# Optimization experiments

Hardware: AMD Instinct MI355X
Metric: run time of the kernel (lower is better)

The kernel has to match this reference:

```python
import jax, jax.numpy as jnp
import numpy as np

EPS = 1e-06        # normalize eps and log eps (module's self.eps)
PDIST_EPS = 1e-06  # torch.nn.PairwiseDistance default eps: ||x1 - x2 + eps||_2

A, C, F = 4096, 8, 64


def setup_inputs() -> dict:
    key = jax.random.key(0)
    x = jax.random.normal(key, (A, C, F), dtype=jnp.float32)
    return {"x": x}


def reference(x) -> jnp.ndarray:
    a = x.shape[0]
    c = x.shape[1]
    # F.normalize(p=2, dim=-1, eps=EPS): x / max(||x||_2, eps)
    nrm = jnp.linalg.norm(x, axis=-1, keepdims=True)
    xn = x / jnp.maximum(nrm, EPS)
    # pairwise cosine similarity per group: [C, A, A]
    sim = jnp.einsum('acf,bcf->cab', xn, xn)
    # mask self-similarity on the diagonal with -1
    diag = jnp.eye(a, dtype=bool)[None, :, :]
    sim = jnp.where(diag, -1.0, sim)
    # nearest neighbor per (c, a): argmax over b -> [C, A] -> [A, C]
    idx = jnp.argmax(sim, axis=-1).T
    # gather matched embeddings: x_match[a, c, f] = xn[idx[a, c], c, f]
    x_match = xn[idx, jnp.arange(c)[None, :], :]
    # PairwiseDistance(p=2, eps=1e-6): ||x - x_match + eps||_2 over last dim
    min_dist = jnp.linalg.norm(xn - x_match + PDIST_EPS, axis=-1)
    loss = -jnp.mean(jnp.log(min_dist + EPS))
    return loss
```

## Files before the change

### kernel.cpp

```cpp
#include <hip/hip_runtime.h>
#include <math.h>

#define AN 4096
#define CN 8
#define FN 64
#define ACN (AN*CN)

typedef __attribute__((ext_vector_type(8))) short bf16x8;
typedef __attribute__((ext_vector_type(4))) float f32x4;

__device__ inline unsigned short f2bf(float f) {
    unsigned u = __float_as_uint(f);
    unsigned r = ((u >> 16) & 1) + 0x7FFFu;
    return (unsigned short)((u + r) >> 16);
}

__global__ __launch_bounds__(256) void k1_normalize(const float* __restrict__ x,
                                                    float* __restrict__ xn,
                                                    unsigned short* __restrict__ xnb)
{
    int tid  = threadIdx.x;
    int grp  = tid >> 4;
    int slot = tid & 15;
    int V = blockIdx.x * 16 + grp;
    const float4 v = *(const float4*)(x + (size_t)V * FN + slot * 4);
    float ss = v.x*v.x + v.y*v.y + v.z*v.z + v.w*v.w;
    ss += __shfl_xor(ss, 1);
    ss += __shfl_xor(ss, 2);
    ss += __shfl_xor(ss, 4);
    ss += __shfl_xor(ss, 8);
    float sc = 1.0f / fmaxf(sqrtf(ss), 1e-6f);
    float4 o; o.x = v.x*sc; o.y = v.y*sc; o.z = v.z*sc; o.w = v.w*sc;
    *(float4*)(xn + (size_t)V * FN + slot * 4) = o;
    int a = V >> 3, c = V & 7;
    ushort4 ob;
    ob.x = f2bf(o.x); ob.y = f2bf(o.y); ob.z = f2bf(o.z); ob.w = f2bf(o.w);
    *(ushort4*)(xnb + ((size_t)c * AN + a) * FN + slot * 4) = ob;
}

__global__ __launch_bounds__(256, 2) void k2_argmax(const unsigned short* __restrict__ xnb,
                                                    unsigned int* __restrict__ pP)
{
    __shared__ uint4 lds4[3 * 1024];

    int blk  = blockIdx.x;
    int half = blk & 1;
    int rt   = (blk >> 1) & 31;
    int c    = blk >> 6;
    int a0   = rt * 128;
    int b0base = half * 2048;

    const uint4* __restrict__ Xc4 = (const uint4*)(xnb + (size_t)c * AN * FN);

    int tid  = threadIdx.x;
    int lane = tid & 63;
    int w    = tid >> 6;
    int wr   = w >> 1;
    int wc   = w & 1;
    int l15  = lane & 15;
    int quad = lane >> 4;

    int srow   = tid >> 3;
    int schunk = tid & 7;

    #pragma unroll
    for (int s = 0; s < 4; ++s) {
        int r = srow + 32 * s;
        lds4[r * 8 + (schunk ^ (r & 7))] = Xc4[(size_t)(a0 + r) * 8 + schunk];
    }
    #pragma unroll
    for (int s = 0; s < 4; ++s) {
        int r = srow + 32 * s;
        lds4[1024 + r * 8 + (schunk ^ (r & 7))] = Xc4[(size_t)(b0base + r) * 8 + schunk];
    }
    __syncthreads();

    bf16x8 afr[4][2];
    #pragma unroll
    for (int mi = 0; mi < 4; ++mi)
        #pragma unroll
        for (int ks = 0; ks < 2; ++ks) {
            int r  = wr * 64 + mi * 16 + l15;
            int ch = (ks * 4 + quad) ^ (r & 7);
            afr[mi][ks] = ((const bf16x8*)lds4)[r * 8 + ch];
        }

    float bestp[16];
    #pragma unroll
    for (int i = 0; i < 16; ++i) bestp[i] = 0.0f;

    const f32x4 two = {2.0f, 2.0f, 2.0f, 2.0f};

    for (int it = 0; it < 16; ++it) {
        int cur = it & 1;
        uint4 gv[4];
        if (it < 15) {
            int g0 = b0base + (it + 1) * 128;
            #pragma unroll
            for (int s = 0; s < 4; ++s)
                gv[s] = Xc4[(size_t)(g0 + srow + 32 * s) * 8 + schunk];
        }

        f32x4 acc[4][4];
        const bf16x8* bt = (const bf16x8*)(lds4 + 1024 + cur * 1024);
        #pragma unroll
        for (int ks = 0; ks < 2; ++ks) {
            #pragma unroll
            for (int ni = 0; ni < 4; ++ni) {
                int r  = wc * 64 + ni * 16 + l15;
                int ch = (ks * 4 + quad) ^ (r & 7);
                bf16x8 bfr = bt[r * 8 + ch];
                #pragma unroll
                for (int mi = 0; mi < 4; ++mi)
                    acc[mi][ni] = __builtin_amdgcn_mfma_f32_16x16x32_bf16(
                        afr[mi][ks], bfr, (ks == 0) ? two : acc[mi][ni], 0, 0, 0);
            }
        }

        int colblk = b0base + it * 128 + wc * 64;
        #pragma unroll
        for (int ni = 0; ni < 4; ++ni) {
            int cfrag = colblk + ni * 16;
            unsigned code = (unsigned)(cfrag + l15);
            #pragma unroll
            for (int mi = 0; mi < 4; ++mi) {
                int rfrag = a0 + wr * 64 + mi * 16;
                bool dg = (rfrag == cfrag);
                #pragma unroll
                for (int r = 0; r < 4; ++r) {
                    unsigned pb = (__float_as_uint(acc[mi][ni][r]) & 0xFFFFF000u) | code;
                    if (dg && (l15 == quad * 4 + r)) pb = 0u;
                    int bi = mi * 4 + r;
                    bestp[bi] = fmaxf(bestp[bi], __uint_as_float(pb));
                }
            }
        }

        if (it < 15) {
            #pragma unroll
            for (int s = 0; s < 4; ++s) {
                int r = srow + 32 * s;
                lds4[1024 + (cur ^ 1) * 1024 + r * 8 + (schunk ^ (r & 7))] = gv[s];
            }
        }
        __syncthreads();
    }

    #pragma unroll
    for (int i = 0; i < 16; ++i) {
        float v = bestp[i];
        v = fmaxf(v, __shfl_xor(v, 1));
        v = fmaxf(v, __shfl_xor(v, 2));
        v = fmaxf(v, __shfl_xor(v, 4));
        v = fmaxf(v, __shfl_xor(v, 8));
        bestp[i] = v;
    }
    __syncthreads();
    float* red = (float*)lds4;
    if (l15 == 0) {
        #pragma unroll
        for (int mi = 0; mi < 4; ++mi)
            #pragma unroll
            for (int r = 0; r < 4; ++r)
                red[w * 64 + mi * 16 + quad * 4 + r] = bestp[mi * 4 + r];
    }
    __syncthreads();
    if (tid < 128) {
        int wr2 = tid >> 6, r64 = tid & 63;
        float p = fmaxf(red[(2 * wr2) * 64 + r64], red[(2 * wr2 + 1) * 64 + r64]);
        int a = a0 + tid;
        pP[(size_t)half * ACN + (size_t)a * CN + c] = __float_as_uint(p);
    }
}

__global__ __launch_bounds__(256) void k3_dist(const float* __restrict__ xn,
                                               const unsigned int* __restrict__ pP,
                                               float* __restrict__ partials)
{
    int id = blockIdx.x * 256 + threadIdx.x;
    float p0 = __uint_as_float(pP[id]);
    float p1 = __uint_as_float(pP[ACN + id]);
    unsigned pm = __float_as_uint(fmaxf(p0, p1));
    int m = (int)(pm & 0xFFFu);
    int c = id & 7;
    const float* xa = xn + (size_t)id * FN;
    const float* xb = xn + ((size_t)m * CN + c) * FN;
    float ss = 0.0f;
    #pragma unroll
    for (int q = 0; q < 16; ++q) {
        float4 va = *(const float4*)(xa + 4 * q);
        float4 vb = *(const float4*)(xb + 4 * q);
        float d0 = va.x - vb.x + 1e-6f;
        float d1 = va.y - vb.y + 1e-6f;
        float d2 = va.z - vb.z + 1e-6f;
        float d3 = va.w - vb.w + 1e-6f;
        ss += d0*d0 + d1*d1 + d2*d2 + d3*d3;
    }
    float val = logf(sqrtf(ss) + 1e-6f);

    float t = val;
    #pragma unroll
    for (int off = 32; off > 0; off >>= 1) t += __shfl_down(t, off);
    __shared__ float ws4[4];
    if ((threadIdx.x & 63) == 0) ws4[threadIdx.x >> 6] = t;
    __syncthreads();
    if (threadIdx.x == 0)
        partials[blockIdx.x] = ws4[0] + ws4[1] + ws4[2] + ws4[3];
}

__global__ __launch_bounds__(64) void k4_final(const float* __restrict__ partials,
                                               float* __restrict__ out)
{
    int t = threadIdx.x;
    float v = partials[t] + partials[t + 64];
    #pragma unroll
    for (int off = 32; off > 0; off >>= 1) v += __shfl_down(v, off);
    if (t == 0) out[0] = -v / (float)ACN;
}

extern "C" void kernel_launch(void* const* d_in, const int* in_sizes, int n_in,
                              void* d_out, int out_size, void* d_ws, size_t ws_size,
                              hipStream_t stream)
{
    const float* x = (const float*)d_in[0];
    float* ws = (float*)d_ws;
    float* xn = ws;
    unsigned short* xnb = (unsigned short*)(xn + (size_t)AN * CN * FN);
    unsigned int* pP = (unsigned int*)(xnb + (size_t)AN * CN * FN);
    float* partials = (float*)(pP + 2 * ACN);

    k1_normalize<<<2048, 256, 0, stream>>>(x, xn, xnb);
    k2_argmax  <<<512, 256, 0, stream>>>(xnb, pP);
    k3_dist    <<<128, 256, 0, stream>>>(xn, pP, partials);
    k4_final   <<<1, 64, 0, stream>>>(partials, (float*)d_out);
}
```

Before: 93.57 us.

## Load MFMA operands straight from global memory and drop the fp32 normalized copy

The argmax kernel no longer stages tiles in LDS with double buffering and per-iteration barriers. Each wave now loads its A and B bf16 fragments directly from global memory (so via L1/L2), fully unrolls the column loop, and masks the diagonal only on the one iteration that holds it. The normalize kernel stops writing the fp32 normalized tensor and stores only a per-row scale, which the distance kernel applies to the raw input, cutting global write traffic. In exchange, B fragments are fetched redundantly from cache by several waves, and the fully unrolled loop raises register pressure.

```diff
diff --git a/kernel.cpp b/kernel.cpp
--- a/kernel.cpp
+++ b/kernel.cpp
@@ -16,8 +16,8 @@
 }
 
 __global__ __launch_bounds__(256) void k1_normalize(const float* __restrict__ x,
-                                                    float* __restrict__ xn,
-                                                    unsigned short* __restrict__ xnb)
+                                                    unsigned short* __restrict__ xnb,
+                                                    float* __restrict__ sc)
 {
     int tid  = threadIdx.x;
     int grp  = tid >> 4;
@@ -29,28 +29,24 @@
     ss += __shfl_xor(ss, 2);
     ss += __shfl_xor(ss, 4);
     ss += __shfl_xor(ss, 8);
-    float sc = 1.0f / fmaxf(sqrtf(ss), 1e-6f);
-    float4 o; o.x = v.x*sc; o.y = v.y*sc; o.z = v.z*sc; o.w = v.w*sc;
-    *(float4*)(xn + (size_t)V * FN + slot * 4) = o;
+    float s = 1.0f / fmaxf(sqrtf(ss), 1e-6f);
+    if (slot == 0) sc[V] = s;
+    ushort4 ob;
+    ob.x = f2bf(v.x * s); ob.y = f2bf(v.y * s);
+    ob.z = f2bf(v.z * s); ob.w = f2bf(v.w * s);
     int a = V >> 3, c = V & 7;
-    ushort4 ob;
-    ob.x = f2bf(o.x); ob.y = f2bf(o.y); ob.z = f2bf(o.z); ob.w = f2bf(o.w);
     *(ushort4*)(xnb + ((size_t)c * AN + a) * FN + slot * 4) = ob;
 }
 
 __global__ __launch_bounds__(256, 2) void k2_argmax(const unsigned short* __restrict__ xnb,
                                                     unsigned int* __restrict__ pP)
 {
-    __shared__ uint4 lds4[3 * 1024];
-
     int blk  = blockIdx.x;
     int half = blk & 1;
     int rt   = (blk >> 1) & 31;
     int c    = blk >> 6;
     int a0   = rt * 128;
     int b0base = half * 2048;
-
-    const uint4* __restrict__ Xc4 = (const uint4*)(xnb + (size_t)c * AN * FN);
 
     int tid  = threadIdx.x;
     int lane = tid & 63;
@@ -60,90 +56,67 @@
     int l15  = lane & 15;
     int quad = lane >> 4;
 
-    int srow   = tid >> 3;
-    int schunk = tid & 7;
-
-    #pragma unroll
-    for (int s = 0; s < 4; ++s) {
-        int r = srow + 32 * s;
-        lds4[r * 8 + (schunk ^ (r & 7))] = Xc4[(size_t)(a0 + r) * 8 + schunk];
-    }
-    #pragma unroll
-    for (int s = 0; s < 4; ++s) {
-        int r = srow + 32 * s;
-        lds4[1024 + r * 8 + (schunk ^ (r & 7))] = Xc4[(size_t)(b0base + r) * 8 + schunk];
-    }
-    __syncthreads();
-
+    const bf16x8* __restrict__ X8 = (const bf16x8*)(xnb + (size_t)c * AN * FN);
+
+    int arow = a0 + wr * 64 + l15;
     bf16x8 afr[4][2];
     #pragma unroll
     for (int mi = 0; mi < 4; ++mi)
         #pragma unroll
-        for (int ks = 0; ks < 2; ++ks) {
-            int r  = wr * 64 + mi * 16 + l15;
-            int ch = (ks * 4 + quad) ^ (r & 7);
-            afr[mi][ks] = ((const bf16x8*)lds4)[r * 8 + ch];
+        for (int ks = 0; ks < 2; ++ks)
+            afr[mi][ks] = X8[(size_t)(arow + mi * 16) * 8 + ks * 4 + quad];
+
+    int row0 = a0 + wr * 64;
+    int rel  = row0 - b0base;
+    int dit  = ((unsigned)rel < 2048u && (((rel >> 6) & 1) == wc)) ? (rel >> 7) : -1;
+    int sdit = __builtin_amdgcn_readfirstlane(dit);
+
+    float bestp[16];
+    #pragma unroll
+    for (int i = 0; i < 16; ++i) bestp[i] = 0.0f;
+
+    const f32x4 two = {2.0f, 2.0f, 2.0f, 2.0f};
+    int bcol = b0base + wc * 64 + l15;
+
+    #pragma unroll
+    for (int it = 0; it < 16; ++it) {
+        bf16x8 bfr[2][4];
+        #pragma unroll
+        for (int ks = 0; ks < 2; ++ks)
+            #pragma unroll
+            for (int ni = 0; ni < 4; ++ni)
+                bfr[ks][ni] = X8[(size_t)(bcol + it * 128 + ni * 16) * 8 + ks * 4 + quad];
+
+        f32x4 acc[4][4];
+        #pragma unroll
+        for (int ni = 0; ni < 4; ++ni)
+            #pragma unroll
+            for (int mi = 0; mi < 4; ++mi) {
+                acc[mi][ni] = __builtin_amdgcn_mfma_f32_16x16x32_bf16(afr[mi][0], bfr[0][ni], two, 0, 0, 0);
+                acc[mi][ni] = __builtin_amdgcn_mfma_f32_16x16x32_bf16(afr[mi][1], bfr[1][ni], acc[mi][ni], 0, 0, 0);
+            }
+
+        if (it == sdit) {
+            #pragma unroll
+            for (int mi = 0; mi < 4; ++mi)
+                #pragma unroll
+                for (int rr = 0; rr < 4; ++rr)
+                    if (l15 == quad * 4 + rr) acc[mi][mi][rr] = -2.0f;
         }
 
-    float bestp[16];
-    #pragma unroll
-    for (int i = 0; i < 16; ++i) bestp[i] = 0.0f;
-
-    const f32x4 two = {2.0f, 2.0f, 2.0f, 2.0f};
-
-    for (int it = 0; it < 16; ++it) {
-        int cur = it & 1;
-        uint4 gv[4];
-        if (it < 15) {
-            int g0 = b0base + (it + 1) * 128;
-            #pragma unroll
-            for (int s = 0; s < 4; ++s)
-                gv[s] = Xc4[(size_t)(g0 + srow + 32 * s) * 8 + schunk];
-        }
-
-        f32x4 acc[4][4];
-        const bf16x8* bt = (const bf16x8*)(lds4 + 1024 + cur * 1024);
-        #pragma unroll
-        for (int ks = 0; ks < 2; ++ks) {
-            #pragma unroll
-            for (int ni = 0; ni < 4; ++ni) {
-                int r  = wc * 64 + ni * 16 + l15;
-                int ch = (ks * 4 + quad) ^ (r & 7);
-                bf16x8 bfr = bt[r * 8 + ch];
-                #pragma unroll
-                for (int mi = 0; mi < 4; ++mi)
-                    acc[mi][ni] = __builtin_amdgcn_mfma_f32_16x16x32_bf16(
-                        afr[mi][ks], bfr, (ks == 0) ? two : acc[mi][ni], 0, 0, 0);
+        int cb = b0base + it * 128 + wc * 64 + l15;
+        #pragma unroll
+        for (int mi = 0; mi < 4; ++mi)
+            #pragma unroll
+            for (int rr = 0; rr < 4; ++rr) {
+                unsigned p0 = (__float_as_uint(acc[mi][0][rr]) & 0xFFFFF000u) | (unsigned)(cb);
+                unsigned p1 = (__float_as_uint(acc[mi][1][rr]) & 0xFFFFF000u) | (unsigned)(cb + 16);
+                unsigned p2 = (__float_as_uint(acc[mi][2][rr]) & 0xFFFFF000u) | (unsigned)(cb + 32);
+                unsigned p3 = (__float_as_uint(acc[mi][3][rr]) & 0xFFFFF000u) | (unsigned)(cb + 48);
+                float m01 = fmaxf(__uint_as_float(p0), __uint_as_float(p1));
+                float m23 = fmaxf(__uint_as_float(p2), __uint_as_float(p3));
+                bestp[mi * 4 + rr] = fmaxf(bestp[mi * 4 + rr], fmaxf(m01, m23));
             }
-        }
-
-        int colblk = b0base + it * 128 + wc * 64;
-        #pragma unroll
-        for (int ni = 0; ni < 4; ++ni) {
-            int cfrag = colblk + ni * 16;
-            unsigned code = (unsigned)(cfrag + l15);
-            #pragma unroll
-            for (int mi = 0; mi < 4; ++mi) {
-                int rfrag = a0 + wr * 64 + mi * 16;
-                bool dg = (rfrag == cfrag);
-                #pragma unroll
-                for (int r = 0; r < 4; ++r) {
-                    unsigned pb = (__float_as_uint(acc[mi][ni][r]) & 0xFFFFF000u) | code;
-                    if (dg && (l15 == quad * 4 + r)) pb = 0u;
-                    int bi = mi * 4 + r;
-                    bestp[bi] = fmaxf(bestp[bi], __uint_as_float(pb));
-                }
-            }
-        }
-
-        if (it < 15) {
-            #pragma unroll
-            for (int s = 0; s < 4; ++s) {
-                int r = srow + 32 * s;
-                lds4[1024 + (cur ^ 1) * 1024 + r * 8 + (schunk ^ (r & 7))] = gv[s];
-            }
-        }
-        __syncthreads();
     }
 
     #pragma unroll
@@ -155,25 +128,25 @@
         v = fmaxf(v, __shfl_xor(v, 8));
         bestp[i] = v;
     }
-    __syncthreads();
-    float* red = (float*)lds4;
+    __shared__ float red[4][64];
     if (l15 == 0) {
         #pragma unroll
         for (int mi = 0; mi < 4; ++mi)
             #pragma unroll
-            for (int r = 0; r < 4; ++r)
-                red[w * 64 + mi * 16 + quad * 4 + r] = bestp[mi * 4 + r];
+            for (int rr = 0; rr < 4; ++rr)
+                red[w][mi * 16 + quad * 4 + rr] = bestp[mi * 4 + rr];
     }
     __syncthreads();
     if (tid < 128) {
         int wr2 = tid >> 6, r64 = tid & 63;
-        float p = fmaxf(red[(2 * wr2) * 64 + r64], red[(2 * wr2 + 1) * 64 + r64]);
-        int a = a0 + tid;
+        float p = fmaxf(red[wr2 * 2][r64], red[wr2 * 2 + 1][r64]);
+        int a = a0 + wr2 * 64 + r64;
         pP[(size_t)half * ACN + (size_t)a * CN + c] = __float_as_uint(p);
     }
 }
 
-__global__ __launch_bounds__(256) void k3_dist(const float* __restrict__ xn,
+__global__ __launch_bounds__(256) void k3_dist(const float* __restrict__ x,
+                                               const float* __restrict__ sc,
                                                const unsigned int* __restrict__ pP,
                                                float* __restrict__ partials)
 {
@@ -183,17 +156,19 @@
     unsigned pm = __float_as_uint(fmaxf(p0, p1));
     int m = (int)(pm & 0xFFFu);
     int c = id & 7;
-    const float* xa = xn + (size_t)id * FN;
-    const float* xb = xn + ((size_t)m * CN + c) * FN;
+    int jb = m * CN + c;
+    float sa = sc[id], sb = sc[jb];
+    const float* xa = x + (size_t)id * FN;
+    const float* xb = x + (size_t)jb * FN;
     float ss = 0.0f;
     #pragma unroll
     for (int q = 0; q < 16; ++q) {
         float4 va = *(const float4*)(xa + 4 * q);
         float4 vb = *(const float4*)(xb + 4 * q);
-        float d0 = va.x - vb.x + 1e-6f;
-        float d1 = va.y - vb.y + 1e-6f;
-        float d2 = va.z - vb.z + 1e-6f;
-        float d3 = va.w - vb.w + 1e-6f;
+        float d0 = va.x * sa - vb.x * sb + 1e-6f;
+        float d1 = va.y * sa - vb.y * sb + 1e-6f;
+        float d2 = va.z * sa - vb.z * sb + 1e-6f;
+        float d3 = va.w * sa - vb.w * sb + 1e-6f;
         ss += d0*d0 + d1*d1 + d2*d2 + d3*d3;
     }
     float val = logf(sqrtf(ss) + 1e-6f);
@@ -223,14 +198,13 @@
                               hipStream_t stream)
 {
     const float* x = (const float*)d_in[0];
-    float* ws = (float*)d_ws;
-    float* xn = ws;
-    unsigned short* xnb = (unsigned short*)(xn + (size_t)AN * CN * FN);
-    unsigned int* pP = (unsigned int*)(xnb + (size_t)AN * CN * FN);
+    unsigned short* xnb = (unsigned short*)d_ws;
+    float* sc = (float*)(xnb + (size_t)AN * CN * FN);
+    unsigned int* pP = (unsigned int*)(sc + ACN);
     float* partials = (float*)(pP + 2 * ACN);
 
-    k1_normalize<<<2048, 256, 0, stream>>>(x, xn, xnb);
+    k1_normalize<<<2048, 256, 0, stream>>>(x, xnb, sc);
     k2_argmax  <<<512, 256, 0, stream>>>(xnb, pP);
-    k3_dist    <<<128, 256, 0, stream>>>(xn, pP, partials);
+    k3_dist    <<<128, 256, 0, stream>>>(x, sc, pP, partials);
     k4_final   <<<1, 64, 0, stream>>>(partials, (float*)d_out);
 }
```

New measurement: 285.4 us. +205.0%, slower.
